# Optimization experiments

Measured on AMD Instinct MI355X. Metric: run time of the kernel, lower is better.

## Reference

```python
import jax, jax.numpy as jnp
import numpy as np

IN_CH = 256
BOT = IN_CH // 2  # bottleneck channels
B, W, H = 4, 64, 64


def setup_inputs() -> dict:
    key = jax.random.key(0)
    ks = jax.random.split(key, 10)
    s_in = 1.0 / np.sqrt(IN_CH)   # torch Conv2d default init scale (kaiming-ish bound)
    s_bt = 1.0 / np.sqrt(BOT)
    return {
        "X": jax.random.normal(ks[0], (B, IN_CH, W, H), dtype=jnp.float32),
        "Wq": jax.random.uniform(ks[1], (BOT, IN_CH), jnp.float32, -s_in, s_in),
        "bq": jax.random.uniform(ks[2], (BOT,), jnp.float32, -s_in, s_in),
        "Wk": jax.random.uniform(ks[3], (BOT, IN_CH), jnp.float32, -s_in, s_in),
        "bk": jax.random.uniform(ks[4], (BOT,), jnp.float32, -s_in, s_in),
        "Wv": jax.random.uniform(ks[5], (BOT, IN_CH), jnp.float32, -s_in, s_in),
        "bv": jax.random.uniform(ks[6], (BOT,), jnp.float32, -s_in, s_in),
        "Wo": jax.random.uniform(ks[7], (IN_CH, BOT), jnp.float32, -s_bt, s_bt),
        "bo": jax.random.uniform(ks[8], (IN_CH,), jnp.float32, -s_bt, s_bt),
        "gamma": 0.1 * jax.random.normal(ks[9], (1,), dtype=jnp.float32),
    }


def reference(X, Wq, bq, Wk, bk, Wv, bv, Wo, bo, gamma):
    b, c, w, h = X.shape
    n = w * h
    Xf = X.reshape(b, c, n)  # [b, c, n] — 1x1 conv == per-pixel linear
    q = jnp.einsum('oc,bcn->bon', Wq, Xf) + bq[None, :, None]  # [b, c/2, n]
    k = jnp.einsum('oc,bcn->bon', Wk, Xf) + bk[None, :, None]
    v = jnp.einsum('oc,bcn->bon', Wv, Xf) + bv[None, :, None]
    # score[b,i,j] = sum_c q[b,c,i] * k[b,c,j]; softmax over dim=1 (query index i)
    score = jnp.einsum('bci,bcj->bij', q, k)          # [b, n, n]
    attn = jax.nn.softmax(score, axis=1)
    out = jnp.einsum('bci,bij->bcj', v, attn)         # [b, c/2, n]
    out = jnp.einsum('oc,bcn->bon', Wo, out) + bo[None, :, None]  # [b, c, n]
    out = out.reshape(b, c, w, h)
    return gamma[0] * out + X
```

## Files before the change

kernel.cpp:

```cpp
#include <hip/hip_runtime.h>
#include <math.h>

#define NBATCH 4
#define CIN    256
#define CBOT   128
#define NPIX   4096
#define NPART  4
#define LOG2E  1.44269504f

typedef __attribute__((ext_vector_type(4))) float f32x4;
typedef __attribute__((ext_vector_type(8))) short bf16x8;

__device__ __forceinline__ unsigned short f2bf(float f) {
    union { float f; unsigned u; } v; v.f = f;
    unsigned r = (v.u + 0x7FFFu + ((v.u >> 16) & 1u)) >> 16;
    return (unsigned short)r;
}
__device__ __forceinline__ unsigned pk2bf(float a, float b) {
#if __has_builtin(__builtin_amdgcn_cvt_pk_bf16_f32)
    auto r = __builtin_amdgcn_cvt_pk_bf16_f32(a, b);
    unsigned u; __builtin_memcpy(&u, &r, 4); return u;
#else
    return (unsigned)f2bf(a) | ((unsigned)f2bf(b) << 16);
#endif
}
__device__ __forceinline__ float fexp2(float x) {
#if __has_builtin(__builtin_amdgcn_exp2f)
    return __builtin_amdgcn_exp2f(x);
#else
    return exp2f(x);
#endif
}

__global__ __launch_bounds__(256) void k_wcvt(
    const float* __restrict__ Wq, const float* __restrict__ Wk,
    const float* __restrict__ Wv, const float* __restrict__ Wo,
    unsigned short* __restrict__ Wb)
{
    const int f4 = (blockIdx.x * 256 + threadIdx.x) * 4;
    const int reg = f4 >> 15, loc = f4 & 32767;
    const float* __restrict__ W = (reg == 0) ? Wq : (reg == 1) ? Wk : (reg == 2) ? Wv : Wo;
    const float sc = (reg == 1) ? LOG2E : 1.f;
    float4 v = *(const float4*)(W + loc);
    uint2 u;
    u.x = pk2bf(v.x * sc, v.y * sc);
    u.y = pk2bf(v.z * sc, v.w * sc);
    *(uint2*)&Wb[f4] = u;
}

__global__ __launch_bounds__(256) void k_qkvx(
    const float* __restrict__ X,
    const unsigned short* __restrict__ Wb,
    const float* __restrict__ bq, const float* __restrict__ bk,
    const float* __restrict__ bv,
    unsigned short* __restrict__ Qt, unsigned short* __restrict__ Kt,
    unsigned short* __restrict__ Vt)
{
    __shared__ __align__(16) unsigned short Xs[32][264];
    const int tid = threadIdx.x;
    const int wv = tid >> 6, lane = tid & 63;
    const int grp = lane & 15, quad = lane >> 4;
    const int pbase = blockIdx.x * 32;
    const int b     = blockIdx.y;
    const float* __restrict__ Xg = X + (size_t)b * CIN * NPIX + pbase;

#pragma unroll
    for (int k = 0; k < 8; ++k) {
        int f = tid + 256 * k;
        int c = f >> 3, pg = (f & 7) << 2;
        float4 v = *(const float4*)(Xg + (size_t)c * NPIX + pg);
        Xs[pg + 0][c] = f2bf(v.x);
        Xs[pg + 1][c] = f2bf(v.y);
        Xs[pg + 2][c] = f2bf(v.z);
        Xs[pg + 3][c] = f2bf(v.w);
    }
    __syncthreads();

    const unsigned short* __restrict__ Wqb = Wb;
    const unsigned short* __restrict__ Wkb = Wb + 32768;
    const unsigned short* __restrict__ Wvb = Wb + 65536;
    const int obase = 32 * wv;

    f32x4 aQ[2][2], aK[2][2], aV[2][2];
#pragma unroll
    for (int mt = 0; mt < 2; ++mt)
#pragma unroll
        for (int nt = 0; nt < 2; ++nt) {
            aQ[mt][nt] = (f32x4)0.f; aK[mt][nt] = (f32x4)0.f; aV[mt][nt] = (f32x4)0.f;
        }

    for (int ks = 0; ks < 8; ++ks) {
        bf16x8 bx[2];
#pragma unroll
        for (int nt = 0; nt < 2; ++nt)
            bx[nt] = *(const bf16x8*)&Xs[nt * 16 + grp][ks * 32 + quad * 8];
        bf16x8 wq_[2], wk_[2], wv_[2];
#pragma unroll
        for (int mt = 0; mt < 2; ++mt) {
            const size_t roff = (size_t)(obase + mt * 16 + grp) * CIN + ks * 32 + quad * 8;
            wq_[mt] = *(const bf16x8*)&Wqb[roff];
            wk_[mt] = *(const bf16x8*)&Wkb[roff];
            wv_[mt] = *(const bf16x8*)&Wvb[roff];
        }
#pragma unroll
        for (int mt = 0; mt < 2; ++mt)
#pragma unroll
            for (int nt = 0; nt < 2; ++nt) {
                aQ[mt][nt] = __builtin_amdgcn_mfma_f32_16x16x32_bf16(wq_[mt], bx[nt], aQ[mt][nt], 0, 0, 0);
                aK[mt][nt] = __builtin_amdgcn_mfma_f32_16x16x32_bf16(wk_[mt], bx[nt], aK[mt][nt], 0, 0, 0);
                aV[mt][nt] = __builtin_amdgcn_mfma_f32_16x16x32_bf16(bx[mt], wv_[nt], aV[mt][nt], 0, 0, 0);
            }
    }

    unsigned short* Qb_ = Qt + (size_t)b * NPIX * CBOT;
    unsigned short* Kb_ = Kt + (size_t)b * NPIX * CBOT;
#pragma unroll
    for (int mt = 0; mt < 2; ++mt) {
        int o0 = obase + mt * 16 + quad * 4;
        float b4q[4], b4k[4];
#pragma unroll
        for (int r = 0; r < 4; ++r) { b4q[r] = bq[o0 + r]; b4k[r] = bk[o0 + r] * LOG2E; }
#pragma unroll
        for (int nt = 0; nt < 2; ++nt) {
            int p = pbase + nt * 16 + grp;
            uint2 uq, uk;
            uq.x = pk2bf(aQ[mt][nt][0] + b4q[0], aQ[mt][nt][1] + b4q[1]);
            uq.y = pk2bf(aQ[mt][nt][2] + b4q[2], aQ[mt][nt][3] + b4q[3]);
            uk.x = pk2bf(aK[mt][nt][0] + b4k[0], aK[mt][nt][1] + b4k[1]);
            uk.y = pk2bf(aK[mt][nt][2] + b4k[2], aK[mt][nt][3] + b4k[3]);
            *(uint2*)&Qb_[(size_t)p * CBOT + o0] = uq;
            *(uint2*)&Kb_[(size_t)p * CBOT + o0] = uk;
        }
    }
    unsigned short* Vb_ = Vt + (size_t)b * CBOT * NPIX;
#pragma unroll
    for (int nt = 0; nt < 2; ++nt) {
        int o = obase + nt * 16 + grp;
        float bb = bv[o];
#pragma unroll
        for (int mt = 0; mt < 2; ++mt) {
            int p0 = pbase + mt * 16 + quad * 4;
            uint2 u;
            u.x = pk2bf(aV[mt][nt][0] + bb, aV[mt][nt][1] + bb);
            u.y = pk2bf(aV[mt][nt][2] + bb, aV[mt][nt][3] + bb);
            *(uint2*)&Vb_[(size_t)o * NPIX + p0] = u;
        }
    }
}

__global__ __launch_bounds__(256, 2) void k_flash(
    const unsigned short* __restrict__ Qt,
    const unsigned short* __restrict__ Kt,
    const unsigned short* __restrict__ Vt,
    unsigned short* __restrict__ Opart,
    float* __restrict__ Lpart)
{
    __shared__ __align__(16) unsigned short Qs[64][136];
    __shared__ __align__(16) unsigned short Vs[128][72];
    __shared__ __align__(16) unsigned short Ps[128][72];
    const int tid  = threadIdx.x;
    const int wv   = tid >> 6, lane = tid & 63;
    const int grp  = lane & 15, quad = lane >> 4;
    const int jblk = blockIdx.x * 128;
    const int part = blockIdx.y;
    const int b    = blockIdx.z;
    const int tbeg = part * (64 / NPART);
    const int tend = tbeg + (64 / NPART);
    const unsigned short* __restrict__ Qb = Qt + (size_t)b * NPIX * CBOT;
    const unsigned short* __restrict__ Kb = Kt + (size_t)b * NPIX * CBOT;
    const unsigned short* __restrict__ Vb = Vt + (size_t)b * CBOT * NPIX;

    bf16x8 aq[2][4];
#pragma unroll
    for (int set = 0; set < 2; ++set)
#pragma unroll
        for (int ks = 0; ks < 4; ++ks)
            aq[set][ks] = *(const bf16x8*)&Kb[
                (size_t)(jblk + wv * 32 + set * 16 + grp) * CBOT + ks * 32 + quad * 8];

    bf16x8 bones;
#pragma unroll
    for (int t = 0; t < 8; ++t) bones[t] = (short)0x3F80;

    f32x4 o[2][8];
#pragma unroll
    for (int set = 0; set < 2; ++set)
#pragma unroll
        for (int ct = 0; ct < 8; ++ct) o[set][ct] = (f32x4)0.f;
    f32x4 lacc[2] = {(f32x4)0.f, (f32x4)0.f};

    const int qrow = tid >> 4, qch = tid & 15;
    const int vrow = tid >> 3, vch = tid & 7;
    bf16x8 qreg[4], vreg[4];
#pragma unroll
    for (int k = 0; k < 4; ++k) {
        qreg[k] = *(const bf16x8*)&Qb[(size_t)(tbeg * 64 + qrow + 16 * k) * CBOT + qch * 8];
        vreg[k] = *(const bf16x8*)&Vb[(size_t)(vrow + 32 * k) * NPIX + tbeg * 64 + vch * 8];
    }

    for (int it = tbeg; it < tend; ++it) {
        __syncthreads();
#pragma unroll
        for (int k = 0; k < 4; ++k) {
            *(bf16x8*)&Qs[qrow + 16 * k][qch * 8] = qreg[k];
            *(bf16x8*)&Vs[vrow + 32 * k][vch * 8] = vreg[k];
        }
        __syncthreads();
        if (it + 1 < tend) {
            const int i1 = (it + 1) * 64;
#pragma unroll
            for (int k = 0; k < 4; ++k) {
                qreg[k] = *(const bf16x8*)&Qb[(size_t)(i1 + qrow + 16 * k) * CBOT + qch * 8];
                vreg[k] = *(const bf16x8*)&Vb[(size_t)(vrow + 32 * k) * NPIX + i1 + vch * 8];
            }
        }

        f32x4 sf[2][4];
#pragma unroll
        for (int set = 0; set < 2; ++set)
#pragma unroll
            for (int nt = 0; nt < 4; ++nt) sf[set][nt] = (f32x4)0.f;
#pragma unroll
        for (int nt = 0; nt < 4; ++nt)
#pragma unroll
            for (int ks = 0; ks < 4; ++ks) {
                bf16x8 bq_ = *(const bf16x8*)&Qs[nt * 16 + grp][ks * 32 + quad * 8];
                sf[0][nt] = __builtin_amdgcn_mfma_f32_16x16x32_bf16(aq[0][ks], bq_, sf[0][nt], 0, 0, 0);
                sf[1][nt] = __builtin_amdgcn_mfma_f32_16x16x32_bf16(aq[1][ks], bq_, sf[1][nt], 0, 0, 0);
            }

#pragma unroll
        for (int set = 0; set < 2; ++set) {
            const int rbase = wv * 32 + set * 16 + quad * 4;
#pragma unroll
            for (int nt = 0; nt < 4; ++nt) {
                const int col = nt * 16 + grp;
                unsigned u01 = pk2bf(fexp2(sf[set][nt][0]), fexp2(sf[set][nt][1]));
                unsigned u23 = pk2bf(fexp2(sf[set][nt][2]), fexp2(sf[set][nt][3]));
                Ps[rbase + 0][col] = (unsigned short)u01;
                Ps[rbase + 1][col] = (unsigned short)(u01 >> 16);
                Ps[rbase + 2][col] = (unsigned short)u23;
                Ps[rbase + 3][col] = (unsigned short)(u23 >> 16);
            }
        }

        bf16x8 af[2][2];
#pragma unroll
        for (int set = 0; set < 2; ++set)
#pragma unroll
            for (int ks2 = 0; ks2 < 2; ++ks2)
                af[set][ks2] = *(const bf16x8*)&Ps[wv * 32 + set * 16 + grp][ks2 * 32 + quad * 8];

#pragma unroll
        for (int ct = 0; ct < 8; ++ct)
#pragma unroll
            for (int ks2 = 0; ks2 < 2; ++ks2) {
                bf16x8 bv_ = *(const bf16x8*)&Vs[ct * 16 + grp][ks2 * 32 + quad * 8];
                o[0][ct] = __builtin_amdgcn_mfma_f32_16x16x32_bf16(af[0][ks2], bv_, o[0][ct], 0, 0, 0);
                o[1][ct] = __builtin_amdgcn_mfma_f32_16x16x32_bf16(af[1][ks2], bv_, o[1][ct], 0, 0, 0);
            }
#pragma unroll
        for (int set = 0; set < 2; ++set) {
            lacc[set] = __builtin_amdgcn_mfma_f32_16x16x32_bf16(af[set][0], bones, lacc[set], 0, 0, 0);
            lacc[set] = __builtin_amdgcn_mfma_f32_16x16x32_bf16(af[set][1], bones, lacc[set], 0, 0, 0);
        }
    }

    unsigned short* Ob = Opart + ((size_t)(part * NBATCH + b) * NPIX + jblk) * CBOT;
#pragma unroll
    for (int set = 0; set < 2; ++set)
#pragma unroll
        for (int ct = 0; ct < 8; ++ct)
#pragma unroll
            for (int r = 0; r < 4; ++r)
                Ob[(size_t)(wv * 32 + set * 16 + quad * 4 + r) * CBOT + ct * 16 + grp] =
                    f2bf(o[set][ct][r]);
    if (grp == 0) {
#pragma unroll
        for (int set = 0; set < 2; ++set)
#pragma unroll
            for (int r = 0; r < 4; ++r)
                Lpart[(size_t)(part * NBATCH + b) * NPIX + jblk + wv * 32 + set * 16 + quad * 4 + r] =
                    lacc[set][r];
    }
}

__global__ __launch_bounds__(256) void k_oproj(
    const unsigned short* __restrict__ Opart, const float* __restrict__ Lpart,
    const unsigned short* __restrict__ Wob, const float* __restrict__ bo,
    const float* __restrict__ gamma, const float* __restrict__ X,
    float* __restrict__ Out)
{
    const int tid = threadIdx.x;
    const int wv = tid >> 6, lane = tid & 63;
    const int grp = lane & 15, quad = lane >> 4;
    const int pbase = blockIdx.x * 32;
    const int b     = blockIdx.y;
    const int obase = 64 * wv;

    f32x4 acc[2][4];
#pragma unroll
    for (int mt = 0; mt < 2; ++mt)
#pragma unroll
        for (int nt = 0; nt < 4; ++nt) acc[mt][nt] = (f32x4)0.f;

    for (int ks = 0; ks < 4; ++ks) {
        bf16x8 bw[4];
#pragma unroll
        for (int nt = 0; nt < 4; ++nt)
            bw[nt] = *(const bf16x8*)&Wob[(size_t)(obase + nt * 16 + grp) * CBOT + ks * 32 + quad * 8];
#pragma unroll
        for (int mt = 0; mt < 2; ++mt) {
            int p = pbase + mt * 16 + grp;
#pragma unroll
            for (int part = 0; part < NPART; ++part) {
                bf16x8 ao = *(const bf16x8*)&Opart[
                    ((size_t)(part * NBATCH + b) * NPIX + p) * CBOT + ks * 32 + quad * 8];
#pragma unroll
                for (int nt = 0; nt < 4; ++nt)
                    acc[mt][nt] = __builtin_amdgcn_mfma_f32_16x16x32_bf16(ao, bw[nt], acc[mt][nt], 0, 0, 0);
            }
        }
    }

    float linv[2][4];
#pragma unroll
    for (int mt = 0; mt < 2; ++mt)
#pragma unroll
        for (int r = 0; r < 4; ++r) {
            int p = pbase + mt * 16 + quad * 4 + r;
            float ls = 0.f;
#pragma unroll
            for (int part = 0; part < NPART; ++part)
                ls += Lpart[(size_t)(part * NBATCH + b) * NPIX + p];
            linv[mt][r] = 1.f / ls;
        }
    float g = gamma[0];
#pragma unroll
    for (int nt = 0; nt < 4; ++nt) {
        int o = obase + nt * 16 + grp;
        float bb = bo[o];
#pragma unroll
        for (int mt = 0; mt < 2; ++mt) {
            int p0 = pbase + mt * 16 + quad * 4;
            size_t base = (size_t)b * CIN * NPIX + (size_t)o * NPIX + p0;
            float4 x4 = *(const float4*)(X + base);
            float4 r4;
            r4.x = g * (acc[mt][nt][0] * linv[mt][0] + bb) + x4.x;
            r4.y = g * (acc[mt][nt][1] * linv[mt][1] + bb) + x4.y;
            r4.z = g * (acc[mt][nt][2] * linv[mt][2] + bb) + x4.z;
            r4.w = g * (acc[mt][nt][3] * linv[mt][3] + bb) + x4.w;
            *(float4*)(Out + base) = r4;
        }
    }
}

extern "C" void kernel_launch(void* const* d_in, const int* in_sizes, int n_in,
                              void* d_out, int out_size, void* d_ws, size_t ws_size,
                              hipStream_t stream)
{
    (void)in_sizes; (void)n_in; (void)out_size; (void)ws_size;
    const float* X     = (const float*)d_in[0];
    const float* Wq    = (const float*)d_in[1];
    const float* bq    = (const float*)d_in[2];
    const float* Wk    = (const float*)d_in[3];
    const float* bk    = (const float*)d_in[4];
    const float* Wv    = (const float*)d_in[5];
    const float* bv    = (const float*)d_in[6];
    const float* Wo    = (const float*)d_in[7];
    const float* bo    = (const float*)d_in[8];
    const float* gamma = (const float*)d_in[9];
    float* out = (float*)d_out;

    const size_t BNC = (size_t)NBATCH * NPIX * CBOT;
    unsigned short* Qt    = (unsigned short*)d_ws;
    unsigned short* Kt    = Qt + BNC;
    unsigned short* Vt    = Kt + BNC;
    unsigned short* Opart = Vt + BNC;
    float*          Lpart = (float*)(Opart + (size_t)NPART * BNC);
    unsigned short* Wb    = (unsigned short*)(Lpart + (size_t)NPART * NBATCH * NPIX);

    k_wcvt <<<dim3(128),               256, 0, stream>>>(Wq, Wk, Wv, Wo, Wb);
    k_qkvx <<<dim3(128, NBATCH),       256, 0, stream>>>(X, Wb, bq, bk, bv, Qt, Kt, Vt);
    k_flash<<<dim3(32, NPART, NBATCH), 256, 0, stream>>>(Qt, Kt, Vt, Opart, Lpart);
    k_oproj<<<dim3(128, NBATCH),       256, 0, stream>>>(Opart, Lpart, Wb + 98304, bo, gamma, X, out);
}
```

Baseline: 161.3 us.

## Keep P in registers via permlane swaps and double-buffer Q/V LDS tiles

The flash kernel now computes the transposed score tile (Q rows as A, K as B), so the exp'd probabilities come out in a layout that permlane32/16 swaps can turn directly into MFMA B-operands. This removes the LDS round trip and barrier for the P matrix. Q and V tiles are double-buffered in dynamic LDS with a two-deep register prefetch, leaving one barrier per iteration instead of two. Output stores also become vectorized 8-byte writes. In exchange, LDS use doubles for Q/V, which may limit occupancy, and the code depends on the permlane swap instructions.

```diff
diff --git a/kernel.cpp b/kernel.cpp
--- a/kernel.cpp
+++ b/kernel.cpp
@@ -29,6 +29,22 @@
     return __builtin_amdgcn_exp2f(x);
 #else
     return exp2f(x);
+#endif
+}
+__device__ __forceinline__ void plswap32(unsigned &a, unsigned &b) {
+#if __has_builtin(__builtin_amdgcn_permlane32_swap)
+    auto r = __builtin_amdgcn_permlane32_swap(a, b, false, false);
+    a = (unsigned)r[0]; b = (unsigned)r[1];
+#else
+    asm volatile("v_permlane32_swap_b32 %0, %1" : "+v"(a), "+v"(b));
+#endif
+}
+__device__ __forceinline__ void plswap16(unsigned &a, unsigned &b) {
+#if __has_builtin(__builtin_amdgcn_permlane16_swap)
+    auto r = __builtin_amdgcn_permlane16_swap(a, b, false, false);
+    a = (unsigned)r[0]; b = (unsigned)r[1];
+#else
+    asm volatile("v_permlane16_swap_b32 %0, %1" : "+v"(a), "+v"(b));
 #endif
 }
 
@@ -155,9 +171,9 @@
     unsigned short* __restrict__ Opart,
     float* __restrict__ Lpart)
 {
-    __shared__ __align__(16) unsigned short Qs[64][136];
-    __shared__ __align__(16) unsigned short Vs[128][72];
-    __shared__ __align__(16) unsigned short Ps[128][72];
+    extern __shared__ __align__(16) unsigned short lds[];
+#define QS(bi, r, c) lds[(bi) * 8704 + (r) * 136 + (c)]
+#define VS(bi, r, c) lds[17408 + (bi) * 9216 + (r) * 72 + (c)]
     const int tid  = threadIdx.x;
     const int wv   = tid >> 6, lane = tid & 63;
     const int grp  = lane & 15, quad = lane >> 4;
@@ -170,23 +186,21 @@
     const unsigned short* __restrict__ Kb = Kt + (size_t)b * NPIX * CBOT;
     const unsigned short* __restrict__ Vb = Vt + (size_t)b * CBOT * NPIX;
 
-    bf16x8 aq[2][4];
-#pragma unroll
-    for (int set = 0; set < 2; ++set)
+    bf16x8 bk[2][4];
+#pragma unroll
+    for (int nt = 0; nt < 2; ++nt)
 #pragma unroll
         for (int ks = 0; ks < 4; ++ks)
-            aq[set][ks] = *(const bf16x8*)&Kb[
-                (size_t)(jblk + wv * 32 + set * 16 + grp) * CBOT + ks * 32 + quad * 8];
-
-    bf16x8 bones;
-#pragma unroll
-    for (int t = 0; t < 8; ++t) bones[t] = (short)0x3F80;
-
-    f32x4 o[2][8];
-#pragma unroll
-    for (int set = 0; set < 2; ++set)
-#pragma unroll
-        for (int ct = 0; ct < 8; ++ct) o[set][ct] = (f32x4)0.f;
+            bk[nt][ks] = *(const bf16x8*)&Kb[
+                (size_t)(jblk + wv * 32 + nt * 16 + grp) * CBOT + ks * 32 + quad * 8];
+
+    bf16x8 aones;
+#pragma unroll
+    for (int t = 0; t < 8; ++t) aones[t] = (short)0x3F80;
+
+    f32x4 o[8][2];
+#pragma unroll
+    for (int ct = 0; ct < 8; ++ct) { o[ct][0] = (f32x4)0.f; o[ct][1] = (f32x4)0.f; }
     f32x4 lacc[2] = {(f32x4)0.f, (f32x4)0.f};
 
     const int qrow = tid >> 4, qch = tid & 15;
@@ -197,92 +211,105 @@
         qreg[k] = *(const bf16x8*)&Qb[(size_t)(tbeg * 64 + qrow + 16 * k) * CBOT + qch * 8];
         vreg[k] = *(const bf16x8*)&Vb[(size_t)(vrow + 32 * k) * NPIX + tbeg * 64 + vch * 8];
     }
+#pragma unroll
+    for (int k = 0; k < 4; ++k) {
+        *(bf16x8*)&QS(0, qrow + 16 * k, qch * 8) = qreg[k];
+        *(bf16x8*)&VS(0, vrow + 32 * k, vch * 8) = vreg[k];
+    }
+    {
+        const int i1 = (tbeg + 1) * 64;
+#pragma unroll
+        for (int k = 0; k < 4; ++k) {
+            qreg[k] = *(const bf16x8*)&Qb[(size_t)(i1 + qrow + 16 * k) * CBOT + qch * 8];
+            vreg[k] = *(const bf16x8*)&Vb[(size_t)(vrow + 32 * k) * NPIX + i1 + vch * 8];
+        }
+    }
+    __syncthreads();
 
     for (int it = tbeg; it < tend; ++it) {
-        __syncthreads();
-#pragma unroll
-        for (int k = 0; k < 4; ++k) {
-            *(bf16x8*)&Qs[qrow + 16 * k][qch * 8] = qreg[k];
-            *(bf16x8*)&Vs[vrow + 32 * k][vch * 8] = vreg[k];
-        }
-        __syncthreads();
+        const int cur = (it - tbeg) & 1;
+
+        f32x4 sf[4][2];
+#pragma unroll
+        for (int mt = 0; mt < 4; ++mt) { sf[mt][0] = (f32x4)0.f; sf[mt][1] = (f32x4)0.f; }
+#pragma unroll
+        for (int mt = 0; mt < 4; ++mt)
+#pragma unroll
+            for (int ks = 0; ks < 4; ++ks) {
+                bf16x8 aq_ = *(const bf16x8*)&QS(cur, mt * 16 + grp, ks * 32 + quad * 8);
+                sf[mt][0] = __builtin_amdgcn_mfma_f32_16x16x32_bf16(aq_, bk[0][ks], sf[mt][0], 0, 0, 0);
+                sf[mt][1] = __builtin_amdgcn_mfma_f32_16x16x32_bf16(aq_, bk[1][ks], sf[mt][1], 0, 0, 0);
+            }
+
         if (it + 1 < tend) {
-            const int i1 = (it + 1) * 64;
 #pragma unroll
             for (int k = 0; k < 4; ++k) {
-                qreg[k] = *(const bf16x8*)&Qb[(size_t)(i1 + qrow + 16 * k) * CBOT + qch * 8];
-                vreg[k] = *(const bf16x8*)&Vb[(size_t)(vrow + 32 * k) * NPIX + i1 + vch * 8];
-            }
-        }
-
-        f32x4 sf[2][4];
-#pragma unroll
-        for (int set = 0; set < 2; ++set)
-#pragma unroll
-            for (int nt = 0; nt < 4; ++nt) sf[set][nt] = (f32x4)0.f;
-#pragma unroll
-        for (int nt = 0; nt < 4; ++nt)
-#pragma unroll
-            for (int ks = 0; ks < 4; ++ks) {
-                bf16x8 bq_ = *(const bf16x8*)&Qs[nt * 16 + grp][ks * 32 + quad * 8];
-                sf[0][nt] = __builtin_amdgcn_mfma_f32_16x16x32_bf16(aq[0][ks], bq_, sf[0][nt], 0, 0, 0);
-                sf[1][nt] = __builtin_amdgcn_mfma_f32_16x16x32_bf16(aq[1][ks], bq_, sf[1][nt], 0, 0, 0);
-            }
-
-#pragma unroll
-        for (int set = 0; set < 2; ++set) {
-            const int rbase = wv * 32 + set * 16 + quad * 4;
-#pragma unroll
-            for (int nt = 0; nt < 4; ++nt) {
-                const int col = nt * 16 + grp;
-                unsigned u01 = pk2bf(fexp2(sf[set][nt][0]), fexp2(sf[set][nt][1]));
-                unsigned u23 = pk2bf(fexp2(sf[set][nt][2]), fexp2(sf[set][nt][3]));
-                Ps[rbase + 0][col] = (unsigned short)u01;
-                Ps[rbase + 1][col] = (unsigned short)(u01 >> 16);
-                Ps[rbase + 2][col] = (unsigned short)u23;
-                Ps[rbase + 3][col] = (unsigned short)(u23 >> 16);
-            }
-        }
-
-        bf16x8 af[2][2];
-#pragma unroll
-        for (int set = 0; set < 2; ++set)
-#pragma unroll
-            for (int ks2 = 0; ks2 < 2; ++ks2)
-                af[set][ks2] = *(const bf16x8*)&Ps[wv * 32 + set * 16 + grp][ks2 * 32 + quad * 8];
+                *(bf16x8*)&QS(cur ^ 1, qrow + 16 * k, qch * 8) = qreg[k];
+                *(bf16x8*)&VS(cur ^ 1, vrow + 32 * k, vch * 8) = vreg[k];
+            }
+            if (it + 2 < tend) {
+                const int i2 = (it + 2) * 64;
+#pragma unroll
+                for (int k = 0; k < 4; ++k) {
+                    qreg[k] = *(const bf16x8*)&Qb[(size_t)(i2 + qrow + 16 * k) * CBOT + qch * 8];
+                    vreg[k] = *(const bf16x8*)&Vb[(size_t)(vrow + 32 * k) * NPIX + i2 + vch * 8];
+                }
+            }
+        }
+
+        bf16x8 pf[2][2];
+#pragma unroll
+        for (int nt = 0; nt < 2; ++nt)
+#pragma unroll
+            for (int h = 0; h < 2; ++h) {
+                unsigned u0a = pk2bf(fexp2(sf[2 * h][nt][0]),     fexp2(sf[2 * h][nt][1]));
+                unsigned u1a = pk2bf(fexp2(sf[2 * h][nt][2]),     fexp2(sf[2 * h][nt][3]));
+                unsigned u0b = pk2bf(fexp2(sf[2 * h + 1][nt][0]), fexp2(sf[2 * h + 1][nt][1]));
+                unsigned u1b = pk2bf(fexp2(sf[2 * h + 1][nt][2]), fexp2(sf[2 * h + 1][nt][3]));
+                plswap32(u0a, u0b); plswap16(u0a, u0b);
+                plswap32(u1a, u1b); plswap16(u1a, u1b);
+                union { unsigned u[4]; bf16x8 v; } cvt;
+                cvt.u[0] = u0a; cvt.u[1] = u1a; cvt.u[2] = u0b; cvt.u[3] = u1b;
+                pf[nt][h] = cvt.v;
+            }
 
 #pragma unroll
         for (int ct = 0; ct < 8; ++ct)
 #pragma unroll
-            for (int ks2 = 0; ks2 < 2; ++ks2) {
-                bf16x8 bv_ = *(const bf16x8*)&Vs[ct * 16 + grp][ks2 * 32 + quad * 8];
-                o[0][ct] = __builtin_amdgcn_mfma_f32_16x16x32_bf16(af[0][ks2], bv_, o[0][ct], 0, 0, 0);
-                o[1][ct] = __builtin_amdgcn_mfma_f32_16x16x32_bf16(af[1][ks2], bv_, o[1][ct], 0, 0, 0);
-            }
-#pragma unroll
-        for (int set = 0; set < 2; ++set) {
-            lacc[set] = __builtin_amdgcn_mfma_f32_16x16x32_bf16(af[set][0], bones, lacc[set], 0, 0, 0);
-            lacc[set] = __builtin_amdgcn_mfma_f32_16x16x32_bf16(af[set][1], bones, lacc[set], 0, 0, 0);
-        }
+            for (int h = 0; h < 2; ++h) {
+                bf16x8 av_ = *(const bf16x8*)&VS(cur, ct * 16 + grp, h * 32 + quad * 8);
+                o[ct][0] = __builtin_amdgcn_mfma_f32_16x16x32_bf16(av_, pf[0][h], o[ct][0], 0, 0, 0);
+                o[ct][1] = __builtin_amdgcn_mfma_f32_16x16x32_bf16(av_, pf[1][h], o[ct][1], 0, 0, 0);
+            }
+#pragma unroll
+        for (int nt = 0; nt < 2; ++nt) {
+            lacc[nt] = __builtin_amdgcn_mfma_f32_16x16x32_bf16(aones, pf[nt][0], lacc[nt], 0, 0, 0);
+            lacc[nt] = __builtin_amdgcn_mfma_f32_16x16x32_bf16(aones, pf[nt][1], lacc[nt], 0, 0, 0);
+        }
+
+        if (it + 1 < tend) __syncthreads();
     }
 
     unsigned short* Ob = Opart + ((size_t)(part * NBATCH + b) * NPIX + jblk) * CBOT;
 #pragma unroll
-    for (int set = 0; set < 2; ++set)
-#pragma unroll
-        for (int ct = 0; ct < 8; ++ct)
-#pragma unroll
-            for (int r = 0; r < 4; ++r)
-                Ob[(size_t)(wv * 32 + set * 16 + quad * 4 + r) * CBOT + ct * 16 + grp] =
-                    f2bf(o[set][ct][r]);
-    if (grp == 0) {
-#pragma unroll
-        for (int set = 0; set < 2; ++set)
-#pragma unroll
-            for (int r = 0; r < 4; ++r)
-                Lpart[(size_t)(part * NBATCH + b) * NPIX + jblk + wv * 32 + set * 16 + quad * 4 + r] =
-                    lacc[set][r];
-    }
+    for (int nt = 0; nt < 2; ++nt) {
+        const size_t jrow = (size_t)(wv * 32 + nt * 16 + grp) * CBOT;
+#pragma unroll
+        for (int ct = 0; ct < 8; ++ct) {
+            uint2 u;
+            u.x = pk2bf(o[ct][nt][0], o[ct][nt][1]);
+            u.y = pk2bf(o[ct][nt][2], o[ct][nt][3]);
+            *(uint2*)&Ob[jrow + ct * 16 + quad * 4] = u;
+        }
+    }
+    if (quad == 0) {
+#pragma unroll
+        for (int nt = 0; nt < 2; ++nt)
+            Lpart[(size_t)(part * NBATCH + b) * NPIX + jblk + wv * 32 + nt * 16 + grp] =
+                lacc[nt][0];
+    }
+#undef QS
+#undef VS
 }
 
 __global__ __launch_bounds__(256) void k_oproj(
@@ -380,8 +407,10 @@
     float*          Lpart = (float*)(Opart + (size_t)NPART * BNC);
     unsigned short* Wb    = (unsigned short*)(Lpart + (size_t)NPART * NBATCH * NPIX);
 
-    k_wcvt <<<dim3(128),               256, 0, stream>>>(Wq, Wk, Wv, Wo, Wb);
-    k_qkvx <<<dim3(128, NBATCH),       256, 0, stream>>>(X, Wb, bq, bk, bv, Qt, Kt, Vt);
-    k_flash<<<dim3(32, NPART, NBATCH), 256, 0, stream>>>(Qt, Kt, Vt, Opart, Lpart);
-    k_oproj<<<dim3(128, NBATCH),       256, 0, stream>>>(Opart, Lpart, Wb + 98304, bo, gamma, X, out);
-}
+    const int flash_lds = 2 * (64 * 136 + 128 * 72) * 2;
+
+    k_wcvt <<<dim3(128),               256, 0,         stream>>>(Wq, Wk, Wv, Wo, Wb);
+    k_qkvx <<<dim3(128, NBATCH),       256, 0,         stream>>>(X, Wb, bq, bk, bv, Qt, Kt, Vt);
+    k_flash<<<dim3(32, NPART, NBATCH), 256, flash_lds, stream>>>(Qt, Kt, Vt, Opart, Lpart);
+    k_oproj<<<dim3(128, NBATCH),       256, 0,         stream>>>(Opart, Lpart, Wb + 98304, bo, gamma, X, out);
+}
```

New measurement: 162.0 us. Within noise of the previous version (+0.4%).
